# Optimization experiments

Hardware: AMD Instinct MI355X
Metric: run time of the kernel (lower is better)

The kernel has to match this reference:

```python
import jax, jax.numpy as jnp
import numpy as np

N = 100000   # nodes
E = 3200000  # edges
G = 512      # graphs in batch
EPS = 1e-5   # batchnorm eps


def _lin(key, fan_in, fan_out):
    return jax.random.normal(key, (fan_in, fan_out), jnp.float32) / np.sqrt(fan_in)


def setup_inputs() -> dict:
    key = jax.random.key(0)
    ks = jax.random.split(key, 12)
    x = jax.random.normal(ks[0], (N, 2), jnp.float32)
    edge_index = jax.random.randint(ks[1], (2, E), 0, N, dtype=jnp.int64)
    batch_index = jnp.sort(jax.random.randint(ks[2], (N,), 0, G, dtype=jnp.int64))
    w = (8, 32, 128)
    return {
        "x": x, "edge_index": edge_index, "batch_index": batch_index,
        "W1": _lin(ks[3], 2, w[0]),   "b1": jnp.zeros((w[0],), jnp.float32),
        "g1": jnp.ones((w[0],), jnp.float32),  "be1": jnp.zeros((w[0],), jnp.float32),
        "W2": _lin(ks[4], w[0], w[1]), "b2": jnp.zeros((w[1],), jnp.float32),
        "g2": jnp.ones((w[1],), jnp.float32),  "be2": jnp.zeros((w[1],), jnp.float32),
        "W3": _lin(ks[5], w[1], w[2]), "b3": jnp.zeros((w[2],), jnp.float32),
        "g3": jnp.ones((w[2],), jnp.float32),  "be3": jnp.zeros((w[2],), jnp.float32),
        "Wl": _lin(ks[6], w[2], 3),    "bl": jnp.zeros((3,), jnp.float32),
    }


def _gcn_norm(edge_index):
    # add self loops, symmetric normalization (PyG GCNConv default)
    loops = jnp.arange(N, dtype=edge_index.dtype)
    src = jnp.concatenate([edge_index[0], loops])
    dst = jnp.concatenate([edge_index[1], loops])
    deg = jax.ops.segment_sum(jnp.ones_like(dst, jnp.float32), dst, num_segments=N)
    dis = jnp.where(deg > 0, jax.lax.rsqrt(jnp.maximum(deg, 1.0)), 0.0)
    norm = dis[src] * dis[dst]  # [E+N]
    return src, dst, norm


def _gcn_conv(h, W, b, src, dst, norm):
    h = h @ W                                   # [N, out]
    msg = h[src] * norm[:, None]                # gather + scale
    return jax.ops.segment_sum(msg, dst, num_segments=N) + b


def _bn(h, g, b):
    # training-mode batchnorm over node dim
    m = jnp.mean(h, axis=0)
    v = jnp.mean(jnp.square(h - m), axis=0)
    return (h - m) * jax.lax.rsqrt(v + EPS) * g + b


def reference(x, edge_index, batch_index, W1, b1, g1, be1, W2, b2, g2, be2,
              W3, b3, g3, be3, Wl, bl):
    src, dst, norm = _gcn_norm(edge_index)
    h = _bn(jax.nn.relu(_gcn_conv(x, W1, b1, src, dst, norm)), g1, be1)
    h = _bn(jax.nn.relu(_gcn_conv(h, W2, b2, src, dst, norm)), g2, be2)
    h = _bn(jax.nn.relu(_gcn_conv(h, W3, b3, src, dst, norm)), g3, be3)
    pooled = jax.ops.segment_max(h, batch_index, num_segments=G)  # [G, 128]
    logits = pooled @ Wl + bl                                     # [G, 3]
    return jax.nn.log_softmax(logits, axis=1)
```

## Files before the change

### kernel.cpp

```cpp
#include <hip/hip_runtime.h>
#include <hip/hip_bf16.h>
#include <hip/hip_fp16.h>
#include <math.h>

#define N_NODES 100000
#define N_EDGES 3200000
#define N_GRAPHS 512
#define BN_EPS 1e-5f
#define NBIN ((N_NODES + 511) / 512)
#define CHUNK 8192
#define NCHUNK ((N_EDGES + CHUNK - 1) / CHUNK)
#define STORE_CAP (N_EDGES + 16 * NBIN * NCHUNK)
#define LSEG 98
#define NSEGB ((N_NODES + LSEG - 1) / LSEG)
#define NSTATB ((N_NODES + 127) / 128)
#define PLANE2 ((size_t)(N_NODES + 1) * 16)
#define PLANEU ((size_t)N_NODES * 16)

typedef _Float16 half8_t __attribute__((ext_vector_type(8)));
typedef float float4_t __attribute__((ext_vector_type(4)));

struct alignas(8) h4 { __half2 a, b; };
struct alignas(16) h8s { __half2 h[4]; };


__global__ void k_hist2(const int* __restrict__ dst, int* __restrict__ hists) {
    __shared__ int h[NBIN];
    for (int i = threadIdx.x; i < NBIN; i += blockDim.x) h[i] = 0;
    __syncthreads();
    int e0 = blockIdx.x * CHUNK;
    int e1 = min(e0 + CHUNK, N_EDGES);
    for (int e = e0 + threadIdx.x; e < e1; e += blockDim.x)
        atomicAdd(&h[dst[e] >> 9], 1);
    __syncthreads();
    for (int i = threadIdx.x; i < NBIN; i += blockDim.x)
        hists[i * NCHUNK + blockIdx.x] = h[i];
}

__global__ void k_scan2(int* __restrict__ hists, int* __restrict__ ghist) {
    int b = blockIdx.x;
    int lane = threadIdx.x;
    int carry = 0;
    int base = b * NCHUNK;
    for (int c0 = 0; c0 < NCHUNK; c0 += 64) {
        int c = c0 + lane;
        int v = (c < NCHUNK) ? hists[base + c] : 0;
        int pv = (v + 15) & ~15;
        int inc = pv;
#pragma unroll
        for (int off = 1; off < 64; off <<= 1) {
            int u = __shfl_up(inc, off, 64);
            if (lane >= off) inc += u;
        }
        if (c < NCHUNK) hists[base + c] = inc - pv + carry;
        carry += __shfl(inc, 63, 64);
    }
    if (lane == 0) ghist[b] = carry;
}

__global__ void k_binscan(const int* __restrict__ ghist, int* __restrict__ bbase) {
    __shared__ int sd[512];
    int t = threadIdx.x;
    int v = (t < NBIN) ? ghist[t] : 0;
    sd[t] = v;
    __syncthreads();
    for (int off = 1; off < 512; off <<= 1) {
        int u = (t >= off) ? sd[t - off] : 0;
        __syncthreads();
        sd[t] += u;
        __syncthreads();
    }
    if (t < NBIN) bbase[t] = sd[t] - v;
    if (t == 511) bbase[NBIN] = sd[511];
}

__global__ void k_scatter(const int* __restrict__ src, const int* __restrict__ dst,
                          const int* __restrict__ bbase, const int* __restrict__ hists,
                          int* __restrict__ store) {
    __shared__ int cur[NBIN];
    for (int i = threadIdx.x; i < NBIN; i += blockDim.x)
        cur[i] = bbase[i] + hists[i * NCHUNK + blockIdx.x];
    __syncthreads();
    int e0 = blockIdx.x * CHUNK;
    int e1 = min(e0 + CHUNK, N_EDGES);
    for (int e = e0 + threadIdx.x; e < e1; e += blockDim.x) {
        int d = dst[e];
        int b = d >> 9;
        int pos = atomicAdd(&cur[b], 1);
        store[pos] = (src[e] << 9) | (d & 511);
    }
    __syncthreads();
    for (int i = threadIdx.x; i < NBIN; i += blockDim.x) {
        int p = cur[i];
        int end = (p + 15) & ~15;
        for (; p < end; ++p) store[p] = -1;
    }
}

__global__ void k_csr_build(const int* __restrict__ bbase, const int* __restrict__ store,
                            const float* __restrict__ x, int* __restrict__ offs,
                            int* __restrict__ ends, float* __restrict__ dis,
                            float* __restrict__ rdis, float4* __restrict__ xd,
                            int* __restrict__ csr) {
    __shared__ int cnt[512], cur[512], wsum[4];
    int b = blockIdx.x;
    int n0 = b << 9;
    int e0 = bbase[b], e1 = bbase[b + 1];
    int t = threadIdx.x;
    int lane = t & 63, wid = t >> 6;
    if (t < 512) cnt[t] = 0;
    __syncthreads();
    for (int e = e0 + t; e < e1; e += 1024) {
        int p = store[e];
        if (p >= 0) atomicAdd(&cnt[p & 511], 1);
    }
    __syncthreads();
    int c0 = 0, c1 = 0, pair = 0, inc = 0;
    if (t < 256) {
        c0 = cnt[2 * t];
        c1 = cnt[2 * t + 1];
        pair = c0 + c1;
        inc = pair;
#pragma unroll
        for (int off = 1; off < 64; off <<= 1) {
            int u = __shfl_up(inc, off, 64);
            if (lane >= off) inc += u;
        }
        if (lane == 63) wsum[wid] = inc;
    }
    __syncthreads();
    if (t < 256) {
        int wo = 0;
        for (int w = 0; w < wid; ++w) wo += wsum[w];
        int ex = inc - pair + wo;
        cur[2 * t] = ex;
        cur[2 * t + 1] = ex + c0;
#pragma unroll
        for (int j = 0; j < 2; ++j) {
            int n = n0 + 2 * t + j;
            int cc = j ? c1 : c0;
            int exx = j ? ex + c0 : ex;
            if (n < N_NODES) {
                offs[n] = e0 + exx;
                ends[n] = e0 + exx + cc;
                float dn = rsqrtf(1.0f + (float)cc);
                dis[n] = dn;
                rdis[n] = sqrtf(1.0f + (float)cc);
                float2 xv = *(const float2*)(x + 2 * (size_t)n);
                xd[n] = make_float4(dn * xv.x, dn * xv.y, dn, 0.f);
            } else if (n == N_NODES) {
                xd[N_NODES] = make_float4(0.f, 0.f, 0.f, 0.f);
            }
        }
    }
    __syncthreads();
    for (int e = e0 + t; e < e1; e += 1024) {
        int p = store[e];
        if (p >= 0) {
            int pos = e0 + atomicAdd(&cur[p & 511], 1);
            csr[pos] = p >> 9;
        }
    }
}


__global__ void k_agg1(const float4* __restrict__ xd, const int* __restrict__ offs,
                       const int* __restrict__ ends, const int* __restrict__ csr,
                       const float* __restrict__ W1, const float* __restrict__ b1,
                       float* __restrict__ svec, __half* __restrict__ ys1) {
    __shared__ float sW[16], sb[8];
    int t = threadIdx.x;
    if (t < 16) sW[t] = W1[t];
    if (t < 8) sb[t] = b1[t];
    __syncthreads();
    int wave = t >> 6, lane = t & 63;
    int nsub = lane >> 4, eg = lane & 15;
    int node = ((blockIdx.x * 4 + wave) << 2) + nsub;
    int e0 = offs[node], e1 = ends[node];
    float ax = 0.f, ay = 0.f, as = 0.f;
    for (int e = e0 + eg; e < e1; e += 32) {
        int s0 = csr[e];
        int s1 = (e + 16 < e1) ? csr[e + 16] : N_NODES;
        float4 v0 = xd[s0];
        float4 v1 = xd[s1];
        ax += v0.x + v1.x;
        ay += v0.y + v1.y;
        as += v0.z + v1.z;
    }
#pragma unroll
    for (int off = 1; off < 16; off <<= 1) {
        ax += __shfl_xor(ax, off, 64);
        ay += __shfl_xor(ay, off, 64);
        as += __shfl_xor(as, off, 64);
    }
    if (eg == 0) {
        float4 xn = xd[node];
        float dn = xn.z;
        float u0x = dn * (ax + xn.x);
        float u0y = dn * (ay + xn.y);
        svec[node] = dn * (as + xn.z);
        float y[8];
#pragma unroll
        for (int f = 0; f < 8; ++f)
            y[f] = dn * fmaxf(u0x * sW[f] + u0y * sW[8 + f] + sb[f], 0.f);
        h8s o;
#pragma unroll
        for (int q = 0; q < 4; ++q) o.h[q] = __floats2half2_rn(y[2 * q], y[2 * q + 1]);
        *(h8s*)(ys1 + (size_t)node * 8) = o;
    }
}


__global__ void k_prep2(const float* __restrict__ stats, const float* __restrict__ gamma,
                        const float* __restrict__ beta, const float* __restrict__ W2,
                        float* __restrict__ W2p, float* __restrict__ cw2,
                        __half* __restrict__ ys1) {
    __shared__ float a1[8], c1[8];
    int t = threadIdx.x;
    if (t < 8) {
        float inv_n = 1.0f / (float)N_NODES;
        float m = stats[t] * inv_n;
        float v = stats[8 + t] * inv_n - m * m;
        float a = gamma[t] * rsqrtf(v + BN_EPS);
        a1[t] = a;
        c1[t] = beta[t] - m * a;
    }
    __syncthreads();
    W2p[t] = a1[t >> 5] * W2[t];
    if (t < 32) {
        float cb = 0.f;
#pragma unroll
        for (int i = 0; i < 8; ++i) cb += c1[i] * W2[i * 32 + t];
        cw2[t] = cb;
    }
    if (t == 128) *(int4*)(ys1 + (size_t)N_NODES * 8) = make_int4(0, 0, 0, 0);
}


__global__ void k_agg2(const __half* __restrict__ ys1, const int* __restrict__ offs,
                       const int* __restrict__ ends, const int* __restrict__ csr,
                       const float* __restrict__ dis, const float* __restrict__ svec,
                       const float* __restrict__ W2p, const float* __restrict__ cw2,
                       const float* __restrict__ b2, __half* __restrict__ ys2) {
    __shared__ float sW[256], sC[32], sB[32];
    int t = threadIdx.x;
    sW[t] = W2p[t];
    if (t < 32) { sC[t] = cw2[t]; sB[t] = b2[t]; }
    __syncthreads();
    int wave = t >> 6, lane = t & 63;
    int nsub = lane >> 3, eg = (lane >> 1) & 3, chunk = lane & 1;
    int node = ((blockIdx.x * 4 + wave) << 3) + nsub;
    int e0 = offs[node], e1 = ends[node];
    float a0 = 0.f, a1 = 0.f, a2 = 0.f, a3 = 0.f;
    const __half* hp = ys1 + chunk * 4;
    for (int e = e0 + eg; e < e1; e += 8) {
        int s0 = csr[e];
        int s1 = (e + 4 < e1) ? csr[e + 4] : N_NODES;
        h4 v0 = *(const h4*)(hp + (size_t)s0 * 8);
        h4 v1 = *(const h4*)(hp + (size_t)s1 * 8);
        a0 += __low2float(v0.a) + __low2float(v1.a);
        a1 += __high2float(v0.a) + __high2float(v1.a);
        a2 += __low2float(v0.b) + __low2float(v1.b);
        a3 += __high2float(v0.b) + __high2float(v1.b);
    }
    if (eg == 0) {
        h4 v = *(const h4*)(hp + (size_t)node * 8);
        a0 += __low2float(v.a);
        a1 += __high2float(v.a);
        a2 += __low2float(v.b);
        a3 += __high2float(v.b);
    }
#pragma unroll
    for (int off = 2; off < 8; off <<= 1) {
        a0 += __shfl_xor(a0, off, 64);
        a1 += __shfl_xor(a1, off, 64);
        a2 += __shfl_xor(a2, off, 64);
        a3 += __shfl_xor(a3, off, 64);
    }
    int lb = nsub << 3;
    float u[8];
    u[0] = __shfl(a0, lb, 64);     u[1] = __shfl(a1, lb, 64);
    u[2] = __shfl(a2, lb, 64);     u[3] = __shfl(a3, lb, 64);
    u[4] = __shfl(a0, lb + 1, 64); u[5] = __shfl(a1, lb + 1, 64);
    u[6] = __shfl(a2, lb + 1, 64); u[7] = __shfl(a3, lb + 1, 64);
    float dn = dis[node];
    float sv = svec[node];
#pragma unroll
    for (int i = 0; i < 8; ++i) u[i] *= dn;
    int c0 = (lane & 7) * 4;
    float y[4];
#pragma unroll
    for (int k = 0; k < 4; ++k) {
        int col = c0 + k;
        float conv = sB[col] + sv * sC[col];
#pragma unroll
        for (int i = 0; i < 8; ++i) conv += u[i] * sW[i * 32 + col];
        y[k] = dn * fmaxf(conv, 0.f);
    }
    h4 o;
    o.a = __floats2half2_rn(y[0], y[1]);
    o.b = __floats2half2_rn(y[2], y[3]);
    *(h4*)(ys2 + (size_t)(c0 >> 4) * PLANE2 + (size_t)node * 16 + (c0 & 15)) = o;
}


__global__ void k_prep3(const float* __restrict__ stats, const float* __restrict__ gamma,
                        const float* __restrict__ beta, const float* __restrict__ W3,
                        __half* __restrict__ wfrag, float* __restrict__ cw3,
                        __half* __restrict__ ys2) {
    __shared__ float a2[32], c2[32];
    int t = threadIdx.x;
    if (t < 32) {
        float inv_n = 1.0f / (float)N_NODES;
        float m = stats[t] * inv_n;
        float v = stats[32 + t] * inv_n - m * m;
        float a = gamma[t] * rsqrtf(v + BN_EPS);
        a2[t] = a;
        c2[t] = beta[t] - m * a;
    }
    __syncthreads();
    {
        int g = t >> 6, kq = (t >> 4) & 3, c = t & 15;
#pragma unroll
        for (int j = 0; j < 8; ++j) {
            int k = kq * 8 + j;
            wfrag[(size_t)t * 8 + j] = __float2half(a2[k] * W3[k * 128 + g * 16 + c]);
        }
    }
    if (t < 128) {
        float cb = 0.f;
#pragma unroll
        for (int k = 0; k < 32; ++k) cb += c2[k] * W3[k * 128 + t];
        cw3[t] = cb;
    }
    if (t >= 480 && t < 496) {
        int idx = t - 480;
        ((__half2*)(ys2 + (size_t)(idx >> 3) * PLANE2 + (size_t)N_NODES * 16))[idx & 7] =
            __half2{__float2half(0.f), __float2half(0.f)};
    }
}


__global__ void k_agg3(const __half* __restrict__ ys2, const int* __restrict__ offs,
                       const int* __restrict__ ends, const int* __restrict__ csr,
                       const float* __restrict__ dis, __half* __restrict__ u2, int plane) {
    int wave = threadIdx.x >> 6;
    int lane = threadIdx.x & 63;
    int nsub = lane >> 5;
    int eg = (lane >> 2) & 7;
    int chunk = lane & 3;
    int node = ((blockIdx.x * 4 + wave) << 1) + nsub;
    int e0 = offs[node], e1 = ends[node];
    float ax = 0.f, ay = 0.f, az = 0.f, aw = 0.f;
    const __half* hp = ys2 + (size_t)plane * PLANE2 + chunk * 4;
    for (int e = e0 + eg; e < e1; e += 32) {
        int s0 = csr[e];
        int s1 = (e + 8 < e1) ? csr[e + 8] : N_NODES;
        int s2 = (e + 16 < e1) ? csr[e + 16] : N_NODES;
        int s3 = (e + 24 < e1) ? csr[e + 24] : N_NODES;
        h4 v0 = *(const h4*)(hp + (size_t)s0 * 16);
        h4 v1 = *(const h4*)(hp + (size_t)s1 * 16);
        h4 v2 = *(const h4*)(hp + (size_t)s2 * 16);
        h4 v3 = *(const h4*)(hp + (size_t)s3 * 16);
        ax += __low2float(v0.a) + __low2float(v1.a) + __low2float(v2.a) + __low2float(v3.a);
        ay += __high2float(v0.a) + __high2float(v1.a) + __high2float(v2.a) + __high2float(v3.a);
        az += __low2float(v0.b) + __low2float(v1.b) + __low2float(v2.b) + __low2float(v3.b);
        aw += __high2float(v0.b) + __high2float(v1.b) + __high2float(v2.b) + __high2float(v3.b);
    }
    if (eg == 0) {
        h4 v = *(const h4*)(hp + (size_t)node * 16);
        ax += __low2float(v.a);
        ay += __high2float(v.a);
        az += __low2float(v.b);
        aw += __high2float(v.b);
    }
#pragma unroll
    for (int off = 4; off < 32; off <<= 1) {
        ax += __shfl_xor(ax, off, 64);
        ay += __shfl_xor(ay, off, 64);
        az += __shfl_xor(az, off, 64);
        aw += __shfl_xor(aw, off, 64);
    }
    if (eg == 0) {
        float dn = dis[node];
        h4 o;
        o.a = __floats2half2_rn(dn * ax, dn * ay);
        o.b = __floats2half2_rn(dn * az, dn * aw);
        *(h4*)(u2 + (size_t)plane * PLANEU + (size_t)node * 16 + chunk * 4) = o;
    }
}


__global__ void k_mm_mfma(const __half* __restrict__ u2, const __half* __restrict__ wfrag,
                          const float* __restrict__ cw3, const float* __restrict__ b3,
                          const float* __restrict__ svec, const float* __restrict__ dis,
                          __half* __restrict__ ys3) {
    int wave = threadIdx.x >> 6;
    int lane = threadIdx.x & 63;
    int n0 = (blockIdx.x * 4 + wave) * 16;
    if (n0 >= N_NODES) return;
    int m = lane & 15;
    int kq = lane >> 4;

    half8_t af = *(const half8_t*)(u2 + (size_t)(kq >> 1) * PLANEU +
                                   (size_t)(n0 + m) * 16 + (kq & 1) * 8);

    float4_t accs[8];
#pragma unroll
    for (int g = 0; g < 8; ++g) {
        float4_t acc = {0.f, 0.f, 0.f, 0.f};
        half8_t bf = *(const half8_t*)(wfrag + (size_t)((g * 4 + kq) * 16 + m) * 8);
        accs[g] = __builtin_amdgcn_mfma_f32_16x16x32_f16(af, bf, acc, 0, 0, 0);
    }
    float sv[4], dn[4];
#pragma unroll
    for (int r = 0; r < 4; ++r) {
        sv[r] = svec[n0 + kq * 4 + r];
        dn[r] = dis[n0 + kq * 4 + r];
    }
#pragma unroll
    for (int g = 0; g < 8; ++g) {
        float cwf = cw3[g * 16 + m];
        float bf3 = b3[g * 16 + m];
#pragma unroll
        for (int r = 0; r < 4; ++r) {
            float y = fmaxf(accs[g][r] + sv[r] * cwf + bf3, 0.f);
            ys3[(size_t)(n0 + kq * 4 + r) * 128 + g * 16 + m] = __float2half(dn[r] * y);
        }
    }
}


template <int FOUT, bool SPLIT>
__global__ void k_stats(const __half* __restrict__ ys, const float* __restrict__ rdis,
                        float* __restrict__ stats) {
    constexpr int GP = 256 / FOUT;
    int f = threadIdx.x % FOUT, g = threadIdx.x / FOUT;
    float s = 0.f, s2 = 0.f;
    for (int n = blockIdx.x * GP + g; n < N_NODES; n += gridDim.x * GP) {
        size_t idx = SPLIT ? ((size_t)(f >> 4) * PLANE2 + (size_t)n * 16 + (f & 15))
                           : ((size_t)n * FOUT + f);
        float v = __half2float(ys[idx]) * rdis[n];
        s += v;
        s2 += v * v;
    }
    __shared__ float ls[256], ls2[256];
    ls[threadIdx.x] = s;
    ls2[threadIdx.x] = s2;
    __syncthreads();
    if (g == 0) {
        for (int gg = 1; gg < GP; ++gg) {
            s += ls[gg * FOUT + f];
            s2 += ls2[gg * FOUT + f];
        }
        atomicAdd(&stats[f], s);
        atomicAdd(&stats[FOUT + f], s2);
    }
}


__global__ void k_stats128(const __half* __restrict__ ys, const float* __restrict__ rdis,
                           float* __restrict__ part) {
    int t = threadIdx.x;
    int chunk = t & 15, row = t >> 4;
    int n0 = blockIdx.x * 128;
    float s[8] = {0, 0, 0, 0, 0, 0, 0, 0};
    float s2[8] = {0, 0, 0, 0, 0, 0, 0, 0};
#pragma unroll
    for (int i = 0; i < 8; ++i) {
        int n = n0 + i * 16 + row;
        if (n < N_NODES) {
            float r = rdis[n];
            h8s v = *(const h8s*)(ys + (size_t)n * 128 + chunk * 8);
#pragma unroll
            for (int q = 0; q < 4; ++q) {
                float v0 = __low2float(v.h[q]) * r;
                float v1 = __high2float(v.h[q]) * r;
                s[2 * q] += v0;  s2[2 * q] += v0 * v0;
                s[2 * q + 1] += v1;  s2[2 * q + 1] += v1 * v1;
            }
        }
    }
#pragma unroll
    for (int off = 16; off < 64; off <<= 1)
#pragma unroll
        for (int j = 0; j < 8; ++j) {
            s[j] += __shfl_xor(s[j], off, 64);
            s2[j] += __shfl_xor(s2[j], off, 64);
        }
    __shared__ float sm[256];
    sm[t] = 0.f;
    __syncthreads();
    if ((t & 63) < 16) {
#pragma unroll
        for (int j = 0; j < 8; ++j) {
            atomicAdd(&sm[chunk * 8 + j], s[j]);
            atomicAdd(&sm[128 + chunk * 8 + j], s2[j]);
        }
    }
    __syncthreads();
    part[(size_t)blockIdx.x * 256 + t] = sm[t];
}

__global__ void k_stats_red(const float* __restrict__ part, float* __restrict__ stats) {
    int i = blockIdx.x;
    int t = threadIdx.x;
    float s = 0.f;
    for (int b = t; b < NSTATB; b += 256) s += part[(size_t)b * 256 + i];
    __shared__ float sm[256];
    sm[t] = s;
    __syncthreads();
    for (int st = 128; st > 0; st >>= 1) {
        if (t < st) sm[t] += sm[t + st];
        __syncthreads();
    }
    if (t == 0) stats[i] = sm[0];
}


__global__ void k_pool1(const __half* __restrict__ ys3, const float* __restrict__ rdis,
                        const int* __restrict__ batch, int* __restrict__ gmax,
                        int* __restrict__ gmin) {
    __shared__ int sb[LSEG];
    __shared__ float sr[LSEG];
    int n0 = blockIdx.x * LSEG;
    int n1 = min(n0 + LSEG, N_NODES);
    int L = n1 - n0;
    int f = threadIdx.x;
    for (int i = f; i < L; i += 128) { sb[i] = batch[n0 + i]; sr[i] = rdis[n0 + i]; }
    __syncthreads();
    if (L <= 0) return;
    int cg = sb[0];
    int mx = 0;
    int mn = 0x7F800000;
    for (int i = 0; i < L; ++i) {
        int g = sb[i];
        if (g != cg) {
            atomicMax(&gmax[cg * 128 + f], mx);
            atomicMin(&gmin[cg * 128 + f], mn);
            cg = g; mx = 0; mn = 0x7F800000;
        }
        float v = __half2float(ys3[(size_t)(n0 + i) * 128 + f]) * sr[i];
        int b = __float_as_int(v);
        mx = max(mx, b);
        mn = min(mn, b);
    }
    atomicMax(&gmax[cg * 128 + f], mx);
    atomicMin(&gmin[cg * 128 + f], mn);
}


__device__ __forceinline__ int lower_bound_dev(const int* __restrict__ a, int val) {
    int lo = 0, hi = N_NODES;
    while (lo < hi) {
        int mid = (lo + hi) >> 1;
        if (a[mid] < val) lo = mid + 1; else hi = mid;
    }
    return lo;
}

__global__ void k_poolhead(const int* __restrict__ gmax, const int* __restrict__ gmin,
                           const int* __restrict__ batch, const float* __restrict__ stats,
                           const float* __restrict__ gamma, const float* __restrict__ beta,
                           const float* __restrict__ Wl, const float* __restrict__ bl,
                           float* __restrict__ out) {
    int g = blockIdx.x;
    int f = threadIdx.x;
    float inv_n = 1.0f / (float)N_NODES;
    float m = stats[f] * inv_n;
    float var = stats[128 + f] * inv_n - m * m;
    float a = gamma[f] * rsqrtf(var + BN_EPS);
    float c = beta[f] - m * a;
    int s = lower_bound_dev(batch, g);
    int e = lower_bound_dev(batch, g + 1);
    float mx = __int_as_float(gmax[g * 128 + f]);
    float mn = __int_as_float(gmin[g * 128 + f]);
    float r;
    if (e > s) r = (a >= 0.f) ? (a * mx + c) : (a * mn + c);
    else r = -INFINITY;
    __shared__ float l[3][128];
    l[0][f] = r * Wl[f * 3 + 0];
    l[1][f] = r * Wl[f * 3 + 1];
    l[2][f] = r * Wl[f * 3 + 2];
    __syncthreads();
    for (int st = 64; st > 0; st >>= 1) {
        if (f < st) {
            l[0][f] += l[0][f + st];
            l[1][f] += l[1][f + st];
            l[2][f] += l[2][f + st];
        }
        __syncthreads();
    }
    if (f == 0) {
        float l0 = l[0][0] + bl[0], l1 = l[1][0] + bl[1], l2 = l[2][0] + bl[2];
        float mxl = fmaxf(l0, fmaxf(l1, l2));
        float lse = mxl + logf(expf(l0 - mxl) + expf(l1 - mxl) + expf(l2 - mxl));
        out[g * 3 + 0] = l0 - lse;
        out[g * 3 + 1] = l1 - lse;
        out[g * 3 + 2] = l2 - lse;
    }
}


extern "C" void kernel_launch(void* const* d_in, const int* in_sizes, int n_in,
                              void* d_out, int out_size, void* d_ws, size_t ws_size,
                              hipStream_t stream) {
    const float* x   = (const float*)d_in[0];
    const int* ei    = (const int*)d_in[1];
    const int* src   = ei;
    const int* dst   = ei + N_EDGES;
    const int* batch = (const int*)d_in[2];
    const float *W1 = (const float*)d_in[3],  *b1 = (const float*)d_in[4];
    const float *g1 = (const float*)d_in[5],  *be1 = (const float*)d_in[6];
    const float *W2 = (const float*)d_in[7],  *b2 = (const float*)d_in[8];
    const float *g2 = (const float*)d_in[9],  *be2 = (const float*)d_in[10];
    const float *W3 = (const float*)d_in[11], *b3 = (const float*)d_in[12];
    const float *g3 = (const float*)d_in[13], *be3 = (const float*)d_in[14];
    const float *Wl = (const float*)d_in[15], *bl = (const float*)d_in[16];
    float* out = (float*)d_out;

    int* base = (int*)d_ws;
    size_t o = 0;
    float* stats1 = (float*)(base + o); o += 256;
    float* stats2 = (float*)(base + o); o += 256;
    float* stats3 = (float*)(base + o); o += 256;
    int* gmax     = base + o; o += (size_t)N_GRAPHS * 128;
    size_t zero_words = o;
    int* gmin     = base + o; o += (size_t)N_GRAPHS * 128;
    int* bbase    = base + o; o += NBIN + 4;
    int* ghist    = base + o; o += NBIN + 4;
    int* hists    = base + o; o += ((size_t)NBIN * NCHUNK + 3) & ~3ULL;
    float* W2p    = (float*)(base + o); o += 256;
    float* cw2    = (float*)(base + o); o += 32;
    __half* wfrag = (__half*)(base + o); o += 2048;
    float* cw3    = (float*)(base + o); o += 128;
    int* offs     = base + o; o += 100000;
    int* ends     = base + o; o += 100000;
    int* store    = base + o; o += STORE_CAP;
    int* csr      = base + o; o += STORE_CAP;
    float* dis    = (float*)(base + o); o += N_NODES;
    float* rdis   = (float*)(base + o); o += N_NODES;
    float* svec   = (float*)(base + o); o += N_NODES;
    float* spart  = (float*)(base + o); o += (size_t)NSTATB * 256;
    float4* xd    = (float4*)(base + o); o += (size_t)(N_NODES + 1) * 4;
    __half* ys1   = (__half*)(base + o); o += (size_t)(N_NODES + 1) * 4;
    __half* ys2   = (__half*)(base + o); o += (size_t)(N_NODES + 1) * 16;
    __half* u2    = (__half*)(base + o); o += (size_t)N_NODES * 16;
    __half* ys3   = (__half*)(base + o); o += (size_t)N_NODES * 64;
    if (ws_size < o * 4) return;

    const int TB = 256;

    hipMemsetAsync(base, 0, zero_words * 4, stream);
    hipMemsetAsync(gmin, 0x7F, (size_t)N_GRAPHS * 128 * 4, stream);

    k_hist2<<<NCHUNK, 1024, 0, stream>>>(dst, hists);
    k_scan2<<<NBIN, 64, 0, stream>>>(hists, ghist);
    k_binscan<<<1, 512, 0, stream>>>(ghist, bbase);
    k_scatter<<<NCHUNK, 1024, 0, stream>>>(src, dst, bbase, hists, store);
    k_csr_build<<<NBIN, 1024, 0, stream>>>(bbase, store, x, offs, ends, dis, rdis, xd, csr);

    k_agg1<<<N_NODES / 16, TB, 0, stream>>>(xd, offs, ends, csr, W1, b1, svec, ys1);
    k_stats<8, false><<<256, 256, 0, stream>>>(ys1, rdis, stats1);
    k_prep2<<<1, 256, 0, stream>>>(stats1, g1, be1, W2, W2p, cw2, ys1);

    k_agg2<<<N_NODES / 32, TB, 0, stream>>>(ys1, offs, ends, csr, dis, svec, W2p, cw2, b2, ys2);
    k_stats<32, true><<<256, 256, 0, stream>>>(ys2, rdis, stats2);
    k_prep3<<<1, 512, 0, stream>>>(stats2, g2, be2, W3, wfrag, cw3, ys2);

    k_agg3<<<N_NODES / 8, TB, 0, stream>>>(ys2, offs, ends, csr, dis, u2, 0);
    k_agg3<<<N_NODES / 8, TB, 0, stream>>>(ys2, offs, ends, csr, dis, u2, 1);
    k_mm_mfma<<<(N_NODES + 63) / 64, 256, 0, stream>>>(u2, wfrag, cw3, b3, svec, dis, ys3);
    k_stats128<<<NSTATB, 256, 0, stream>>>(ys3, rdis, spart);
    k_stats_red<<<256, 256, 0, stream>>>(spart, stats3);

    k_pool1<<<NSEGB, 128, 0, stream>>>(ys3, rdis, batch, gmax, gmin);
    k_poolhead<<<N_GRAPHS, 128, 0, stream>>>(gmax, gmin, batch, stats3, g3, be3, Wl, bl, out);
}
```

Baseline: 374.5 us.

## Fuse BN statistics into agg2 and MFMA epilogues; deepen gather unrolling

Batchnorm sum and sum-of-squares for layers 2 and 3 are now computed inside the agg2 and MFMA epilogues from unscaled fp32 values. Per-block partials go to a buffer, and small reduction kernels combine them. This removes the separate passes that re-read ys2 and ys3 from memory. The edge-gather loops in agg1, agg2 and agg3 are also unrolled further, issuing 4–8 independent loads per iteration to raise memory-level parallelism. The cost is more register pressure and shared-memory atomics in the epilogues, and the statistics now come from fp32 rather than half-rounded values.

```diff
diff --git a/kernel.cpp b/kernel.cpp
--- a/kernel.cpp
+++ b/kernel.cpp
@@ -13,7 +13,9 @@
 #define STORE_CAP (N_EDGES + 16 * NBIN * NCHUNK)
 #define LSEG 98
 #define NSEGB ((N_NODES + LSEG - 1) / LSEG)
-#define NSTATB ((N_NODES + 127) / 128)
+#define NMMB ((N_NODES + 63) / 64)
+#define NB2 3125
+#define NB2P 3136
 #define PLANE2 ((size_t)(N_NODES + 1) * 16)
 #define PLANEU ((size_t)N_NODES * 16)
 
@@ -178,14 +180,20 @@
     int node = ((blockIdx.x * 4 + wave) << 2) + nsub;
     int e0 = offs[node], e1 = ends[node];
     float ax = 0.f, ay = 0.f, as = 0.f;
-    for (int e = e0 + eg; e < e1; e += 32) {
-        int s0 = csr[e];
-        int s1 = (e + 16 < e1) ? csr[e + 16] : N_NODES;
-        float4 v0 = xd[s0];
-        float4 v1 = xd[s1];
-        ax += v0.x + v1.x;
-        ay += v0.y + v1.y;
-        as += v0.z + v1.z;
+    for (int e = e0 + eg; e < e1; e += 64) {
+        int s[4];
+#pragma unroll
+        for (int j = 0; j < 4; ++j)
+            s[j] = (e + 16 * j < e1) ? csr[e + 16 * j] : N_NODES;
+        float4 v[4];
+#pragma unroll
+        for (int j = 0; j < 4; ++j) v[j] = xd[s[j]];
+#pragma unroll
+        for (int j = 0; j < 4; ++j) {
+            ax += v[j].x;
+            ay += v[j].y;
+            as += v[j].z;
+        }
     }
 #pragma unroll
     for (int off = 1; off < 16; off <<= 1) {
@@ -241,11 +249,13 @@
                        const int* __restrict__ ends, const int* __restrict__ csr,
                        const float* __restrict__ dis, const float* __restrict__ svec,
                        const float* __restrict__ W2p, const float* __restrict__ cw2,
-                       const float* __restrict__ b2, __half* __restrict__ ys2) {
-    __shared__ float sW[256], sC[32], sB[32];
+                       const float* __restrict__ b2, __half* __restrict__ ys2,
+                       float* __restrict__ part2) {
+    __shared__ float sW[256], sC[32], sB[32], sm2[64];
     int t = threadIdx.x;
     sW[t] = W2p[t];
     if (t < 32) { sC[t] = cw2[t]; sB[t] = b2[t]; }
+    if (t < 64) sm2[t] = 0.f;
     __syncthreads();
     int wave = t >> 6, lane = t & 63;
     int nsub = lane >> 3, eg = (lane >> 1) & 3, chunk = lane & 1;
@@ -253,15 +263,21 @@
     int e0 = offs[node], e1 = ends[node];
     float a0 = 0.f, a1 = 0.f, a2 = 0.f, a3 = 0.f;
     const __half* hp = ys1 + chunk * 4;
-    for (int e = e0 + eg; e < e1; e += 8) {
-        int s0 = csr[e];
-        int s1 = (e + 4 < e1) ? csr[e + 4] : N_NODES;
-        h4 v0 = *(const h4*)(hp + (size_t)s0 * 8);
-        h4 v1 = *(const h4*)(hp + (size_t)s1 * 8);
-        a0 += __low2float(v0.a) + __low2float(v1.a);
-        a1 += __high2float(v0.a) + __high2float(v1.a);
-        a2 += __low2float(v0.b) + __low2float(v1.b);
-        a3 += __high2float(v0.b) + __high2float(v1.b);
+    for (int e = e0 + eg; e < e1; e += 16) {
+        int s[4];
+#pragma unroll
+        for (int j = 0; j < 4; ++j)
+            s[j] = (e + 4 * j < e1) ? csr[e + 4 * j] : N_NODES;
+        h4 v[4];
+#pragma unroll
+        for (int j = 0; j < 4; ++j) v[j] = *(const h4*)(hp + (size_t)s[j] * 8);
+#pragma unroll
+        for (int j = 0; j < 4; ++j) {
+            a0 += __low2float(v[j].a);
+            a1 += __high2float(v[j].a);
+            a2 += __low2float(v[j].b);
+            a3 += __high2float(v[j].b);
+        }
     }
     if (eg == 0) {
         h4 v = *(const h4*)(hp + (size_t)node * 8);
@@ -288,19 +304,55 @@
 #pragma unroll
     for (int i = 0; i < 8; ++i) u[i] *= dn;
     int c0 = (lane & 7) * 4;
-    float y[4];
+    float hh[4], hs2[4];
 #pragma unroll
     for (int k = 0; k < 4; ++k) {
         int col = c0 + k;
         float conv = sB[col] + sv * sC[col];
 #pragma unroll
         for (int i = 0; i < 8; ++i) conv += u[i] * sW[i * 32 + col];
-        y[k] = dn * fmaxf(conv, 0.f);
+        hh[k] = fmaxf(conv, 0.f);
+        hs2[k] = hh[k] * hh[k];
     }
     h4 o;
-    o.a = __floats2half2_rn(y[0], y[1]);
-    o.b = __floats2half2_rn(y[2], y[3]);
+    o.a = __floats2half2_rn(dn * hh[0], dn * hh[1]);
+    o.b = __floats2half2_rn(dn * hh[2], dn * hh[3]);
     *(h4*)(ys2 + (size_t)(c0 >> 4) * PLANE2 + (size_t)node * 16 + (c0 & 15)) = o;
+
+    float hs[4];
+#pragma unroll
+    for (int k = 0; k < 4; ++k) hs[k] = hh[k];
+#pragma unroll
+    for (int off = 8; off < 64; off <<= 1)
+#pragma unroll
+        for (int k = 0; k < 4; ++k) {
+            hs[k] += __shfl_xor(hs[k], off, 64);
+            hs2[k] += __shfl_xor(hs2[k], off, 64);
+        }
+    if (nsub == 0) {
+#pragma unroll
+        for (int k = 0; k < 4; ++k) {
+            atomicAdd(&sm2[c0 + k], hs[k]);
+            atomicAdd(&sm2[32 + c0 + k], hs2[k]);
+        }
+    }
+    __syncthreads();
+    if (t < 64) part2[(size_t)t * NB2P + blockIdx.x] = sm2[t];
+}
+
+__global__ void k_red32(const float* __restrict__ part2, float* __restrict__ stats2) {
+    int i = blockIdx.x;
+    int t = threadIdx.x;
+    float s = 0.f;
+    for (int b = t; b < NB2; b += 256) s += part2[(size_t)i * NB2P + b];
+    __shared__ float sm[256];
+    sm[t] = s;
+    __syncthreads();
+    for (int st = 128; st > 0; st >>= 1) {
+        if (t < st) sm[t] += sm[t + st];
+        __syncthreads();
+    }
+    if (t == 0) stats2[i] = sm[0];
 }
 
 
@@ -353,19 +405,21 @@
     int e0 = offs[node], e1 = ends[node];
     float ax = 0.f, ay = 0.f, az = 0.f, aw = 0.f;
     const __half* hp = ys2 + (size_t)plane * PLANE2 + chunk * 4;
-    for (int e = e0 + eg; e < e1; e += 32) {
-        int s0 = csr[e];
-        int s1 = (e + 8 < e1) ? csr[e + 8] : N_NODES;
-        int s2 = (e + 16 < e1) ? csr[e + 16] : N_NODES;
-        int s3 = (e + 24 < e1) ? csr[e + 24] : N_NODES;
-        h4 v0 = *(const h4*)(hp + (size_t)s0 * 16);
-        h4 v1 = *(const h4*)(hp + (size_t)s1 * 16);
-        h4 v2 = *(const h4*)(hp + (size_t)s2 * 16);
-        h4 v3 = *(const h4*)(hp + (size_t)s3 * 16);
-        ax += __low2float(v0.a) + __low2float(v1.a) + __low2float(v2.a) + __low2float(v3.a);
-        ay += __high2float(v0.a) + __high2float(v1.a) + __high2float(v2.a) + __high2float(v3.a);
-        az += __low2float(v0.b) + __low2float(v1.b) + __low2float(v2.b) + __low2float(v3.b);
-        aw += __high2float(v0.b) + __high2float(v1.b) + __high2float(v2.b) + __high2float(v3.b);
+    for (int e = e0 + eg; e < e1; e += 64) {
+        int s[8];
+#pragma unroll
+        for (int j = 0; j < 8; ++j)
+            s[j] = (e + 8 * j < e1) ? csr[e + 8 * j] : N_NODES;
+        h4 v[8];
+#pragma unroll
+        for (int j = 0; j < 8; ++j) v[j] = *(const h4*)(hp + (size_t)s[j] * 16);
+#pragma unroll
+        for (int j = 0; j < 8; ++j) {
+            ax += __low2float(v[j].a);
+            ay += __high2float(v[j].a);
+            az += __low2float(v[j].b);
+            aw += __high2float(v[j].b);
+        }
     }
     if (eg == 0) {
         h4 v = *(const h4*)(hp + (size_t)node * 16);
@@ -394,53 +448,76 @@
 __global__ void k_mm_mfma(const __half* __restrict__ u2, const __half* __restrict__ wfrag,
                           const float* __restrict__ cw3, const float* __restrict__ b3,
                           const float* __restrict__ svec, const float* __restrict__ dis,
-                          __half* __restrict__ ys3) {
-    int wave = threadIdx.x >> 6;
-    int lane = threadIdx.x & 63;
+                          __half* __restrict__ ys3, float* __restrict__ spart) {
+    __shared__ float sm[256];
+    int t = threadIdx.x;
+    int wave = t >> 6;
+    int lane = t & 63;
     int n0 = (blockIdx.x * 4 + wave) * 16;
-    if (n0 >= N_NODES) return;
+    bool active = n0 < N_NODES;
     int m = lane & 15;
     int kq = lane >> 4;
-
-    half8_t af = *(const half8_t*)(u2 + (size_t)(kq >> 1) * PLANEU +
-                                   (size_t)(n0 + m) * 16 + (kq & 1) * 8);
-
-    float4_t accs[8];
-#pragma unroll
-    for (int g = 0; g < 8; ++g) {
-        float4_t acc = {0.f, 0.f, 0.f, 0.f};
-        half8_t bf = *(const half8_t*)(wfrag + (size_t)((g * 4 + kq) * 16 + m) * 8);
-        accs[g] = __builtin_amdgcn_mfma_f32_16x16x32_f16(af, bf, acc, 0, 0, 0);
-    }
-    float sv[4], dn[4];
-#pragma unroll
-    for (int r = 0; r < 4; ++r) {
-        sv[r] = svec[n0 + kq * 4 + r];
-        dn[r] = dis[n0 + kq * 4 + r];
-    }
-#pragma unroll
-    for (int g = 0; g < 8; ++g) {
-        float cwf = cw3[g * 16 + m];
-        float bf3 = b3[g * 16 + m];
+    float ss[8] = {0, 0, 0, 0, 0, 0, 0, 0};
+    float ss2[8] = {0, 0, 0, 0, 0, 0, 0, 0};
+
+    if (active) {
+        half8_t af = *(const half8_t*)(u2 + (size_t)(kq >> 1) * PLANEU +
+                                       (size_t)(n0 + m) * 16 + (kq & 1) * 8);
+        float4_t accs[8];
+#pragma unroll
+        for (int g = 0; g < 8; ++g) {
+            float4_t acc = {0.f, 0.f, 0.f, 0.f};
+            half8_t bf = *(const half8_t*)(wfrag + (size_t)((g * 4 + kq) * 16 + m) * 8);
+            accs[g] = __builtin_amdgcn_mfma_f32_16x16x32_f16(af, bf, acc, 0, 0, 0);
+        }
+        float sv[4], dn[4];
 #pragma unroll
         for (int r = 0; r < 4; ++r) {
-            float y = fmaxf(accs[g][r] + sv[r] * cwf + bf3, 0.f);
-            ys3[(size_t)(n0 + kq * 4 + r) * 128 + g * 16 + m] = __float2half(dn[r] * y);
-        }
-    }
-}
-
-
-template <int FOUT, bool SPLIT>
+            sv[r] = svec[n0 + kq * 4 + r];
+            dn[r] = dis[n0 + kq * 4 + r];
+        }
+#pragma unroll
+        for (int g = 0; g < 8; ++g) {
+            float cwf = cw3[g * 16 + m];
+            float bf3 = b3[g * 16 + m];
+#pragma unroll
+            for (int r = 0; r < 4; ++r) {
+                float y = fmaxf(accs[g][r] + sv[r] * cwf + bf3, 0.f);
+                ss[g] += y;
+                ss2[g] += y * y;
+                ys3[(size_t)(n0 + kq * 4 + r) * 128 + g * 16 + m] = __float2half(dn[r] * y);
+            }
+        }
+    }
+#pragma unroll
+    for (int off = 16; off < 64; off <<= 1)
+#pragma unroll
+        for (int g = 0; g < 8; ++g) {
+            ss[g] += __shfl_xor(ss[g], off, 64);
+            ss2[g] += __shfl_xor(ss2[g], off, 64);
+        }
+    sm[t] = 0.f;
+    __syncthreads();
+    if (active && kq == 0) {
+#pragma unroll
+        for (int g = 0; g < 8; ++g) {
+            atomicAdd(&sm[g * 16 + m], ss[g]);
+            atomicAdd(&sm[128 + g * 16 + m], ss2[g]);
+        }
+    }
+    __syncthreads();
+    spart[(size_t)blockIdx.x * 256 + t] = sm[t];
+}
+
+
+template <int FOUT>
 __global__ void k_stats(const __half* __restrict__ ys, const float* __restrict__ rdis,
                         float* __restrict__ stats) {
     constexpr int GP = 256 / FOUT;
     int f = threadIdx.x % FOUT, g = threadIdx.x / FOUT;
     float s = 0.f, s2 = 0.f;
     for (int n = blockIdx.x * GP + g; n < N_NODES; n += gridDim.x * GP) {
-        size_t idx = SPLIT ? ((size_t)(f >> 4) * PLANE2 + (size_t)n * 16 + (f & 15))
-                           : ((size_t)n * FOUT + f);
-        float v = __half2float(ys[idx]) * rdis[n];
+        float v = __half2float(ys[(size_t)n * FOUT + f]) * rdis[n];
         s += v;
         s2 += v * v;
     }
@@ -458,55 +535,11 @@
     }
 }
 
-
-__global__ void k_stats128(const __half* __restrict__ ys, const float* __restrict__ rdis,
-                           float* __restrict__ part) {
-    int t = threadIdx.x;
-    int chunk = t & 15, row = t >> 4;
-    int n0 = blockIdx.x * 128;
-    float s[8] = {0, 0, 0, 0, 0, 0, 0, 0};
-    float s2[8] = {0, 0, 0, 0, 0, 0, 0, 0};
-#pragma unroll
-    for (int i = 0; i < 8; ++i) {
-        int n = n0 + i * 16 + row;
-        if (n < N_NODES) {
-            float r = rdis[n];
-            h8s v = *(const h8s*)(ys + (size_t)n * 128 + chunk * 8);
-#pragma unroll
-            for (int q = 0; q < 4; ++q) {
-                float v0 = __low2float(v.h[q]) * r;
-                float v1 = __high2float(v.h[q]) * r;
-                s[2 * q] += v0;  s2[2 * q] += v0 * v0;
-                s[2 * q + 1] += v1;  s2[2 * q + 1] += v1 * v1;
-            }
-        }
-    }
-#pragma unroll
-    for (int off = 16; off < 64; off <<= 1)
-#pragma unroll
-        for (int j = 0; j < 8; ++j) {
-            s[j] += __shfl_xor(s[j], off, 64);
-            s2[j] += __shfl_xor(s2[j], off, 64);
-        }
-    __shared__ float sm[256];
-    sm[t] = 0.f;
-    __syncthreads();
-    if ((t & 63) < 16) {
-#pragma unroll
-        for (int j = 0; j < 8; ++j) {
-            atomicAdd(&sm[chunk * 8 + j], s[j]);
-            atomicAdd(&sm[128 + chunk * 8 + j], s2[j]);
-        }
-    }
-    __syncthreads();
-    part[(size_t)blockIdx.x * 256 + t] = sm[t];
-}
-
 __global__ void k_stats_red(const float* __restrict__ part, float* __restrict__ stats) {
     int i = blockIdx.x;
     int t = threadIdx.x;
     float s = 0.f;
-    for (int b = t; b < NSTATB; b += 256) s += part[(size_t)b * 256 + i];
+    for (int b = t; b < NMMB; b += 256) s += part[(size_t)b * 256 + i];
     __shared__ float sm[256];
     sm[t] = s;
     __syncthreads();
@@ -641,7 +674,8 @@
     float* dis    = (float*)(base + o); o += N_NODES;
     float* rdis   = (float*)(base + o); o += N_NODES;
     float* svec   = (float*)(base + o); o += N_NODES;
-    float* spart  = (float*)(base + o); o += (size_t)NSTATB * 256;
+    float* spart  = (float*)(base + o); o += (size_t)NMMB * 256;
+    float* part2  = (float*)(base + o); o += (size_t)64 * NB2P;
     float4* xd    = (float4*)(base + o); o += (size_t)(N_NODES + 1) * 4;
     __half* ys1   = (__half*)(base + o); o += (size_t)(N_NODES + 1) * 4;
     __half* ys2   = (__half*)(base + o); o += (size_t)(N_NODES + 1) * 16;
@@ -661,17 +695,16 @@
     k_csr_build<<<NBIN, 1024, 0, stream>>>(bbase, store, x, offs, ends, dis, rdis, xd, csr);
 
     k_agg1<<<N_NODES / 16, TB, 0, stream>>>(xd, offs, ends, csr, W1, b1, svec, ys1);
-    k_stats<8, false><<<256, 256, 0, stream>>>(ys1, rdis, stats1);
+    k_stats<8><<<256, 256, 0, stream>>>(ys1, rdis, stats1);
     k_prep2<<<1, 256, 0, stream>>>(stats1, g1, be1, W2, W2p, cw2, ys1);
 
-    k_agg2<<<N_NODES / 32, TB, 0, stream>>>(ys1, offs, ends, csr, dis, svec, W2p, cw2, b2, ys2);
-    k_stats<32, true><<<256, 256, 0, stream>>>(ys2, rdis, stats2);
+    k_agg2<<<NB2, TB, 0, stream>>>(ys1, offs, ends, csr, dis, svec, W2p, cw2, b2, ys2, part2);
+    k_red32<<<64, 256, 0, stream>>>(part2, stats2);
     k_prep3<<<1, 512, 0, stream>>>(stats2, g2, be2, W3, wfrag, cw3, ys2);
 
     k_agg3<<<N_NODES / 8, TB, 0, stream>>>(ys2, offs, ends, csr, dis, u2, 0);
     k_agg3<<<N_NODES / 8, TB, 0, stream>>>(ys2, offs, ends, csr, dis, u2, 1);
-    k_mm_mfma<<<(N_NODES + 63) / 64, 256, 0, stream>>>(u2, wfrag, cw3, b3, svec, dis, ys3);
-    k_stats128<<<NSTATB, 256, 0, stream>>>(ys3, rdis, spart);
+    k_mm_mfma<<<NMMB, 256, 0, stream>>>(u2, wfrag, cw3, b3, svec, dis, ys3, spart);
     k_stats_red<<<256, 256, 0, stream>>>(spart, stats3);
 
     k_pool1<<<NSEGB, 128, 0, stream>>>(ys3, rdis, batch, gmax, gmin);
```

After: 359.2 us. 1.04x faster.
